# Kernel optimization log

Hardware: AMD Instinct MI355X
Metric: run time of the kernel (lower is better)

Reference implementation:

```python
import jax, jax.numpy as jnp
import numpy as np

N = 20000       # nodes
E = 160000      # edges (avg degree 8)
NFEAT = 512
NHID = 512
NCLASS = 64
NLAYERS = 4


def setup_inputs() -> dict:
    key = jax.random.key(0)
    ks = jax.random.split(key, 9)
    s = 0.05
    x = jax.random.normal(ks[0], (N, NFEAT), dtype=jnp.float32)
    edge_index = jax.random.randint(ks[1], (2, E), 0, N, dtype=jnp.int64)
    W_enc = jax.random.normal(ks[2], (NFEAT, NHID), dtype=jnp.float32) * s
    b_enc = jnp.zeros((NHID,), dtype=jnp.float32)
    W_convs = jax.random.normal(ks[3], (NLAYERS, NHID, NHID), dtype=jnp.float32) * s
    b_convs = jnp.zeros((NLAYERS, NHID), dtype=jnp.float32)
    W_dec = jax.random.normal(ks[4], (NHID, NCLASS), dtype=jnp.float32) * s
    b_dec = jnp.zeros((NCLASS,), dtype=jnp.float32)
    return {"x": x, "edge_index": edge_index, "W_enc": W_enc, "b_enc": b_enc,
            "W_convs": W_convs, "b_convs": b_convs, "W_dec": W_dec, "b_dec": b_dec}


def reference(x, edge_index, W_enc, b_enc, W_convs, b_convs, W_dec, b_dec):
    n = x.shape[0]
    loops = jnp.arange(n, dtype=edge_index.dtype)
    # GCNConv adds self-loops, then sym-normalizes: D^-1/2 (A+I) D^-1/2
    src = jnp.concatenate([edge_index[0], loops])  # [E+N]
    dst = jnp.concatenate([edge_index[1], loops])  # [E+N]
    deg = jax.ops.segment_sum(jnp.ones_like(dst, dtype=x.dtype), dst, num_segments=N)
    dinv = jnp.where(deg > 0, jax.lax.rsqrt(deg), jnp.zeros_like(deg))
    norm = (dinv[src] * dinv[dst])[:, None]  # [E+N, 1]

    # encoder: relu(Linear)
    h = jax.nn.relu(x @ W_enc + b_enc)

    def gcn_step(h, wb):
        W, b = wb
        hW = h @ W                                   # [N, H]
        msg = hW[src] * norm                         # gather + scale
        agg = jax.ops.segment_sum(msg, dst, num_segments=N)  # scatter-add
        return jax.nn.relu(agg + b), None            # bias after aggregation (PyG)

    h, _ = jax.lax.scan(gcn_step, h, (W_convs, b_convs))

    # decoder (dropout p=0 in eval -> identity)
    return h @ W_dec + b_dec
```

## Files before the change

kernel.cpp:

```cpp
#include <hip/hip_runtime.h>

#define N_NODES 20000
#define E_EDGES 160000
#define NFEAT   512
#define NHID    512
#define NCLASS  64
#define NLAYERS 4

#define SCAN_CHUNK 1024
#define NBLK ((N_NODES + SCAN_CHUNK - 1) / SCAN_CHUNK)
#define CNT_BLOCKS ((E_EDGES + 255) / 256)

using bf16x8 = __attribute__((ext_vector_type(8))) short;
using f32x4  = __attribute__((ext_vector_type(4))) float;
using u16x8  = __attribute__((ext_vector_type(8))) unsigned short;

__device__ __forceinline__ unsigned short f2bf(float f) {
    union { float f; unsigned int u; } v; v.f = f;
    unsigned int u = v.u + 0x7FFFu + ((v.u >> 16) & 1u);
    return (unsigned short)(u >> 16);
}
__device__ __forceinline__ float bf2f(unsigned short h) {
    union { unsigned int u; float f; } v; v.u = ((unsigned int)h) << 16;
    return v.f;
}
__device__ __forceinline__ void gl2lds16(const void* gptr, void* lptr) {
    __builtin_amdgcn_global_load_lds(
        (const __attribute__((address_space(1))) unsigned int*)gptr,
        (__attribute__((address_space(3))) unsigned int*)lptr,
        16, 0, 0);
}

__global__ __launch_bounds__(256) void prep_all(const int* __restrict__ dst,
                                                int* __restrict__ counts,
                                                int* __restrict__ bsums,
                                                const float* __restrict__ W_enc,
                                                const float* __restrict__ W_convs,
                                                const float* __restrict__ W_dec,
                                                unsigned short* __restrict__ WencT,
                                                unsigned short* __restrict__ WcvT,
                                                unsigned short* __restrict__ WdecT) {
    __shared__ int bins[NBLK];
    __shared__ float tile[32][33];
    const int b = blockIdx.x, t = threadIdx.x;

    if (b < CNT_BLOCKS) {
        if (t < NBLK) bins[t] = 0;
        __syncthreads();
        const int e = b * 256 + t;
        if (e < E_EDGES) {
            const int d = dst[e];
            atomicAdd(&counts[d], 1);
            atomicAdd(&bins[d >> 10], 1);
        }
        __syncthreads();
        if (t < NBLK && bins[t]) atomicAdd(&bsums[t], bins[t]);
        return;
    }

    const int bid = b - CNT_BLOCKS;
    const int id  = bid >> 8;
    const int rem = bid & 255;
    const int n0  = (rem & 15) * 32;
    const int k0  = (rem >> 4) * 32;
    const float* W; unsigned short* WT; int N;
    const int K = 512;
    if (id == 0)            { W = W_enc; WT = WencT; N = NHID; }
    else if (id <= NLAYERS) { W = W_convs + (size_t)(id - 1) * NHID * NHID;
                              WT = WcvT  + (size_t)(id - 1) * NHID * NHID; N = NHID; }
    else                    { W = W_dec; WT = WdecT; N = NCLASS; }
    if (n0 >= N) return;
    const int tx = t & 31, ty = t >> 5;
#pragma unroll
    for (int i = 0; i < 32; i += 8)
        tile[ty + i][tx] = W[(size_t)(k0 + ty + i) * N + n0 + tx];
    __syncthreads();
#pragma unroll
    for (int i = 0; i < 32; i += 8)
        WT[(size_t)(n0 + ty + i) * K + k0 + tx] = f2bf(tile[tx][ty + i]);
}

__global__ __launch_bounds__(64) void scan_bsums(const int* __restrict__ bsums,
                                                 int* __restrict__ boffs) {
    const int t = threadIdx.x;
    const int orig = (t < NBLK) ? bsums[t] : 0;
    int v = orig;
    for (int off = 1; off < 64; off <<= 1) {
        int u = __shfl_up(v, off, 64);
        if (t >= off) v += u;
    }
    if (t < NBLK) boffs[t] = v - orig;
}

__global__ __launch_bounds__(256) void write_rowptr(const int* __restrict__ counts,
                                                    const int* __restrict__ boffs,
                                                    int* __restrict__ row_ptr,
                                                    int* __restrict__ cursor,
                                                    float* __restrict__ dinv) {
    __shared__ int part[256];
    const int b = blockIdx.x, t = threadIdx.x;
    const int base = b * SCAN_CHUNK + t * 4;
    int c[4], s = 0;
    for (int i = 0; i < 4; ++i) {
        int idx = base + i;
        c[i] = (idx < N_NODES) ? counts[idx] : 0;
        s += c[i];
    }
    part[t] = s;
    __syncthreads();
    for (int off = 1; off < 256; off <<= 1) {
        int v = (t >= off) ? part[t - off] : 0;
        __syncthreads();
        part[t] += v;
        __syncthreads();
    }
    int run = boffs[b] + ((t == 0) ? 0 : part[t - 1]);
    for (int i = 0; i < 4; ++i) {
        int idx = base + i;
        if (idx < N_NODES) {
            row_ptr[idx] = run;
            cursor[idx]  = run;
            dinv[idx]    = rsqrtf((float)c[i] + 1.0f);
            run += c[i];
        }
    }
    if (b == 0 && t == 0) row_ptr[N_NODES] = E_EDGES;
}

__global__ __launch_bounds__(256) void csr_fill(const int* __restrict__ src,
                                                const int* __restrict__ dst,
                                                const float* __restrict__ dinv,
                                                int* __restrict__ cursor,
                                                int2* __restrict__ ew) {
    int e = blockIdx.x * 256 + threadIdx.x;
    if (e < E_EDGES) {
        int s = src[e], d = dst[e];
        int pos = atomicAdd(&cursor[d], 1);
        ew[pos] = make_int2(s, __float_as_int(dinv[s] * dinv[d]));
    }
    if (e < 8) ew[E_EDGES + e] = make_int2(0, 0);
}

template <int BM, int BN, int WR, int WC, bool RELU, bool HASBIAS, bool OUTBF16, bool A32>
__global__ __launch_bounds__(256) void gemm_mfma(const void* __restrict__ Aptr,
                                                 const unsigned short* __restrict__ BT,
                                                 const float* __restrict__ bias,
                                                 void* __restrict__ Cout,
                                                 int M, int N, int K) {
    constexpr int BK = 32;
    constexpr int R  = BM / (16 * WR);
    constexpr int C  = BN / (16 * WC);
    constexpr int RA = (BM * BK) / (256 * 8);
    constexpr int RB = (BN * BK) / (256 * 8);
    __shared__ unsigned short lA[BM * BK];
    __shared__ unsigned short lB[BN * BK];

    const int t    = threadIdx.x;
    const int lane = t & 63;
    const int wv   = t >> 6;
    const int wr   = wv / WC;
    const int wc   = wv % WC;
    const int lm   = lane & 15;
    const int quad = lane >> 4;

    const int MBLK = (M + BM - 1) / BM;
    const int NBN  = N / BN;
    int mblk, nblk;
    {
        const int i    = blockIdx.x;
        const int full = (MBLK / 8) * 8 * NBN;
        if (i < full) {
            const int g = i / (8 * NBN);
            const int l = i % (8 * NBN);
            mblk = g * 8 + (l & 7);
            nblk = l >> 3;
        } else {
            const int t2  = i - full;
            const int rem = MBLK - (MBLK / 8) * 8;
            mblk = (MBLK / 8) * 8 + t2 % rem;
            nblk = t2 / rem;
        }
    }
    const int m0 = mblk * BM;
    const int n0 = nblk * BN;

    f32x4 acc[R][C] = {};

    for (int kt = 0; kt < K; kt += BK) {
#pragma unroll
        for (int i = 0; i < RA; ++i) {
            int idx = i * 256 + t;
            int row = idx >> 2;
            int kof = (idx & 3) << 3;
            int gr = m0 + row; if (gr >= M) gr = M - 1;
            if constexpr (!A32) {
                gl2lds16((const unsigned short*)Aptr + (size_t)gr * K + kt + kof,
                         &lA[idx * 8]);
            } else {
                const float* p = (const float*)Aptr + (size_t)gr * K + kt + kof;
                float4 f0 = *(const float4*)p;
                float4 f1 = *(const float4*)(p + 4);
                u16x8 pk;
                pk[0] = f2bf(f0.x); pk[1] = f2bf(f0.y);
                pk[2] = f2bf(f0.z); pk[3] = f2bf(f0.w);
                pk[4] = f2bf(f1.x); pk[5] = f2bf(f1.y);
                pk[6] = f2bf(f1.z); pk[7] = f2bf(f1.w);
                *(u16x8*)&lA[idx * 8] = pk;
            }
        }
#pragma unroll
        for (int i = 0; i < RB; ++i) {
            int idx = i * 256 + t;
            int row = idx >> 2;
            int kof = (idx & 3) << 3;
            gl2lds16(BT + (size_t)(n0 + row) * K + kt + kof, &lB[idx * 8]);
        }
        __syncthreads();

        bf16x8 af[R], bfr[C];
#pragma unroll
        for (int r = 0; r < R; ++r)
            af[r] = *(const bf16x8*)&lA[(wr * R * 16 + r * 16 + lm) * BK + quad * 8];
#pragma unroll
        for (int c = 0; c < C; ++c)
            bfr[c] = *(const bf16x8*)&lB[(wc * C * 16 + c * 16 + lm) * BK + quad * 8];
#pragma unroll
        for (int r = 0; r < R; ++r)
#pragma unroll
            for (int c = 0; c < C; ++c)
                acc[r][c] = __builtin_amdgcn_mfma_f32_16x16x32_bf16(af[r], bfr[c],
                                                                    acc[r][c], 0, 0, 0);
        __syncthreads();
    }

#pragma unroll
    for (int r = 0; r < R; ++r) {
#pragma unroll
        for (int c = 0; c < C; ++c) {
            const int colg = n0 + wc * C * 16 + c * 16 + lm;
            const float bb = HASBIAS ? bias[colg] : 0.0f;
            const int rowb = m0 + wr * R * 16 + r * 16 + quad * 4;
#pragma unroll
            for (int i = 0; i < 4; ++i) {
                const int rr = rowb + i;
                if (rr < M) {
                    float v = acc[r][c][i] + bb;
                    if (RELU) v = fmaxf(v, 0.0f);
                    if (OUTBF16)
                        ((unsigned short*)Cout)[(size_t)rr * N + colg] = f2bf(v);
                    else
                        ((float*)Cout)[(size_t)rr * N + colg] = v;
                }
            }
        }
    }
}

__global__ __launch_bounds__(256) void gcn_aggregate(const unsigned short* __restrict__ hW,
                                                     const int* __restrict__ row_ptr,
                                                     const int2* __restrict__ ew,
                                                     const float* __restrict__ dinv,
                                                     const float* __restrict__ bias,
                                                     unsigned short* __restrict__ out) {
    const int wv   = threadIdx.x >> 6;
    const int lane = threadIdx.x & 63;
    int d = blockIdx.x * 4 + wv;
    d = __builtin_amdgcn_readfirstlane(d);
    if (d >= N_NODES) return;
    const int beg = __builtin_amdgcn_readfirstlane(row_ptr[d]);
    const int end = __builtin_amdgcn_readfirstlane(row_ptr[d + 1]);
    const size_t foff = (size_t)lane * 8;

    const float di = dinv[d];
    const float sl = di * di;
    u16x8 sv = *(const u16x8*)(hW + (size_t)d * NHID + foff);
    float acc[8];
#pragma unroll
    for (int i = 0; i < 8; ++i) acc[i] = bf2f(sv[i]) * sl;

    for (int j = beg; j < end; j += 8) {
        int   sK[8];
        float wK[8];
        u16x8 v[8];
#pragma unroll
        for (int k = 0; k < 8; ++k) {
            const int jj = j + k;
            const int2 e = ew[jj];
            const bool valid = jj < end;
            sK[k] = valid ? e.x : 0;
            wK[k] = valid ? __int_as_float(e.y) : 0.0f;
        }
#pragma unroll
        for (int k = 0; k < 8; ++k)
            v[k] = *(const u16x8*)(hW + (size_t)sK[k] * NHID + foff);
#pragma unroll
        for (int k = 0; k < 8; ++k)
#pragma unroll
            for (int i = 0; i < 8; ++i)
                acc[i] += bf2f(v[k][i]) * wK[k];
    }

    const float4 b0v = *(const float4*)(bias + foff);
    const float4 b1v = *(const float4*)(bias + foff + 4);
    u16x8 r;
    r[0] = f2bf(fmaxf(acc[0] + b0v.x, 0.0f));
    r[1] = f2bf(fmaxf(acc[1] + b0v.y, 0.0f));
    r[2] = f2bf(fmaxf(acc[2] + b0v.z, 0.0f));
    r[3] = f2bf(fmaxf(acc[3] + b0v.w, 0.0f));
    r[4] = f2bf(fmaxf(acc[4] + b1v.x, 0.0f));
    r[5] = f2bf(fmaxf(acc[5] + b1v.y, 0.0f));
    r[6] = f2bf(fmaxf(acc[6] + b1v.z, 0.0f));
    r[7] = f2bf(fmaxf(acc[7] + b1v.w, 0.0f));
    *(u16x8*)(out + (size_t)d * NHID + foff) = r;
}

extern "C" void kernel_launch(void* const* d_in, const int* in_sizes, int n_in,
                              void* d_out, int out_size, void* d_ws, size_t ws_size,
                              hipStream_t stream) {
    const float* x       = (const float*)d_in[0];
    const int*   ei      = (const int*)d_in[1];
    const float* W_enc   = (const float*)d_in[2];
    const float* b_enc   = (const float*)d_in[3];
    const float* W_convs = (const float*)d_in[4];
    const float* b_convs = (const float*)d_in[5];
    const float* W_dec   = (const float*)d_in[6];
    const float* b_dec   = (const float*)d_in[7];
    float* out = (float*)d_out;

    const int* src = ei;
    const int* dst = ei + E_EDGES;

    char* ws = (char*)d_ws;
    auto alloc = [&](size_t bytes) {
        char* p = ws;
        ws += (bytes + 255) / 256 * 256;
        return p;
    };
    float* dinv     = (float*)alloc(N_NODES * 4);
    int*   counts   = (int*)  alloc((N_NODES + NBLK) * 4);
    int*   bsums    = counts + N_NODES;
    int*   row_ptr  = (int*)  alloc((N_NODES + 1) * 4);
    int*   cursor   = (int*)  alloc(N_NODES * 4);
    int*   boffs    = (int*)  alloc(NBLK * 4);
    int2*  ew       = (int2*) alloc((E_EDGES + 8) * 8);
    unsigned short* WencT = (unsigned short*)alloc((size_t)NFEAT * NHID * 2);
    unsigned short* WcvT  = (unsigned short*)alloc((size_t)NLAYERS * NHID * NHID * 2);
    unsigned short* WdecT = (unsigned short*)alloc((size_t)NHID * NCLASS * 2);
    unsigned short* B1    = (unsigned short*)alloc((size_t)N_NODES * NHID * 2);
    unsigned short* B2    = (unsigned short*)alloc((size_t)N_NODES * NHID * 2);

    hipMemsetAsync(counts, 0, (N_NODES + NBLK) * sizeof(int), stream);
    prep_all<<<CNT_BLOCKS + 6 * 256, 256, 0, stream>>>(
        dst, counts, bsums, W_enc, W_convs, W_dec, WencT, WcvT, WdecT);
    scan_bsums<<<1, 64, 0, stream>>>(bsums, boffs);
    write_rowptr<<<NBLK, 256, 0, stream>>>(counts, boffs, row_ptr, cursor, dinv);
    csr_fill<<<(E_EDGES + 255) / 256, 256, 0, stream>>>(src, dst, dinv, cursor, ew);

    const int MBLK64 = (N_NODES + 63) / 64;

    gemm_mfma<64, 128, 2, 2, true, true, true, true>
        <<<MBLK64 * (NHID / 128), 256, 0, stream>>>(
        x, WencT, b_enc, B1, N_NODES, NHID, NFEAT);

    for (int L = 0; L < NLAYERS; ++L) {
        gemm_mfma<64, 128, 2, 2, false, false, true, false>
            <<<MBLK64 * (NHID / 128), 256, 0, stream>>>(
            B1, WcvT + (size_t)L * NHID * NHID, nullptr, B2, N_NODES, NHID, NHID);
        gcn_aggregate<<<(N_NODES + 3) / 4, 256, 0, stream>>>(
            B2, row_ptr, ew, dinv, b_convs + (size_t)L * NHID, B1);
    }

    gemm_mfma<64, 64, 2, 2, false, true, false, false>
        <<<MBLK64 * (NCLASS / 64), 256, 0, stream>>>(
        B1, WdecT, b_dec, out, N_NODES, NCLASS, NHID);
}
```

Baseline: 340.7 us.

## Double-buffer GEMM LDS tiles and pre-convert x to bf16 in prep kernel

The MFMA GEMM now uses two LDS buffers and issues the global-to-LDS loads for the next K tile before computing the current one. It uses explicit vmcnt waits and raw s_barrier in place of __syncthreads, so memory latency can overlap with MFMA work. The encoder's fp32 A input is now converted to bf16 once, in extra blocks of the prep kernel, into the B2 scratch buffer. This lets every GEMM take the async-load path without converting in the inner loop. The cost is twice the LDS per block, which may lower occupancy, plus an extra pass over x and fragile hand-written wait counts.

```diff
diff --git a/kernel.cpp b/kernel.cpp
--- a/kernel.cpp
+++ b/kernel.cpp
@@ -10,6 +10,7 @@
 #define SCAN_CHUNK 1024
 #define NBLK ((N_NODES + SCAN_CHUNK - 1) / SCAN_CHUNK)
 #define CNT_BLOCKS ((E_EDGES + 255) / 256)
+#define CVT_BLOCKS ((N_NODES * NFEAT) / 2048)
 
 using bf16x8 = __attribute__((ext_vector_type(8))) short;
 using f32x4  = __attribute__((ext_vector_type(4))) float;
@@ -39,7 +40,9 @@
                                                 const float* __restrict__ W_dec,
                                                 unsigned short* __restrict__ WencT,
                                                 unsigned short* __restrict__ WcvT,
-                                                unsigned short* __restrict__ WdecT) {
+                                                unsigned short* __restrict__ WdecT,
+                                                const float* __restrict__ x,
+                                                unsigned short* __restrict__ Xbf) {
     __shared__ int bins[NBLK];
     __shared__ float tile[32][33];
     const int b = blockIdx.x, t = threadIdx.x;
@@ -55,6 +58,20 @@
         }
         __syncthreads();
         if (t < NBLK && bins[t]) atomicAdd(&bsums[t], bins[t]);
+        return;
+    }
+
+    if (b >= CNT_BLOCKS + 6 * 256) {
+        const int cid = b - CNT_BLOCKS - 6 * 256;
+        const size_t base = (size_t)cid * 2048 + (size_t)t * 8;
+        const float4 f0 = *(const float4*)(x + base);
+        const float4 f1 = *(const float4*)(x + base + 4);
+        u16x8 pk;
+        pk[0] = f2bf(f0.x); pk[1] = f2bf(f0.y);
+        pk[2] = f2bf(f0.z); pk[3] = f2bf(f0.w);
+        pk[4] = f2bf(f1.x); pk[5] = f2bf(f1.y);
+        pk[6] = f2bf(f1.z); pk[7] = f2bf(f1.w);
+        *(u16x8*)(Xbf + base) = pk;
         return;
     }
 
@@ -141,19 +158,20 @@
     if (e < 8) ew[E_EDGES + e] = make_int2(0, 0);
 }
 
-template <int BM, int BN, int WR, int WC, bool RELU, bool HASBIAS, bool OUTBF16, bool A32>
-__global__ __launch_bounds__(256) void gemm_mfma(const void* __restrict__ Aptr,
+template <int BM, int BN, int WR, int WC, bool RELU, bool HASBIAS, bool OUTBF16>
+__global__ __launch_bounds__(256) void gemm_mfma(const unsigned short* __restrict__ A,
                                                  const unsigned short* __restrict__ BT,
                                                  const float* __restrict__ bias,
                                                  void* __restrict__ Cout,
                                                  int M, int N, int K) {
-    constexpr int BK = 32;
-    constexpr int R  = BM / (16 * WR);
-    constexpr int C  = BN / (16 * WC);
-    constexpr int RA = (BM * BK) / (256 * 8);
-    constexpr int RB = (BN * BK) / (256 * 8);
-    __shared__ unsigned short lA[BM * BK];
-    __shared__ unsigned short lB[BN * BK];
+    constexpr int BK  = 32;
+    constexpr int R   = BM / (16 * WR);
+    constexpr int C   = BN / (16 * WC);
+    constexpr int RA  = (BM * BK) / (256 * 8);
+    constexpr int RB  = (BN * BK) / (256 * 8);
+    constexpr int LPT = RA + RB;
+    __shared__ unsigned short lA[2][BM * BK];
+    __shared__ unsigned short lB[2][BN * BK];
 
     const int t    = threadIdx.x;
     const int lane = t & 63;
@@ -186,51 +204,54 @@
 
     f32x4 acc[R][C] = {};
 
-    for (int kt = 0; kt < K; kt += BK) {
+    auto stage = [&](int s, int kt) {
 #pragma unroll
         for (int i = 0; i < RA; ++i) {
             int idx = i * 256 + t;
             int row = idx >> 2;
             int kof = (idx & 3) << 3;
             int gr = m0 + row; if (gr >= M) gr = M - 1;
-            if constexpr (!A32) {
-                gl2lds16((const unsigned short*)Aptr + (size_t)gr * K + kt + kof,
-                         &lA[idx * 8]);
-            } else {
-                const float* p = (const float*)Aptr + (size_t)gr * K + kt + kof;
-                float4 f0 = *(const float4*)p;
-                float4 f1 = *(const float4*)(p + 4);
-                u16x8 pk;
-                pk[0] = f2bf(f0.x); pk[1] = f2bf(f0.y);
-                pk[2] = f2bf(f0.z); pk[3] = f2bf(f0.w);
-                pk[4] = f2bf(f1.x); pk[5] = f2bf(f1.y);
-                pk[6] = f2bf(f1.z); pk[7] = f2bf(f1.w);
-                *(u16x8*)&lA[idx * 8] = pk;
-            }
+            gl2lds16(A + (size_t)gr * K + kt + kof, &lA[s][idx * 8]);
         }
 #pragma unroll
         for (int i = 0; i < RB; ++i) {
             int idx = i * 256 + t;
             int row = idx >> 2;
             int kof = (idx & 3) << 3;
-            gl2lds16(BT + (size_t)(n0 + row) * K + kt + kof, &lB[idx * 8]);
-        }
-        __syncthreads();
+            gl2lds16(BT + (size_t)(n0 + row) * K + kt + kof, &lB[s][idx * 8]);
+        }
+    };
+
+    stage(0, 0);
+    int cur = 0;
+    for (int kt = 0; kt < K; kt += BK) {
+        if (kt + BK < K) {
+            stage(cur ^ 1, kt + BK);
+            asm volatile("s_waitcnt vmcnt(%0)" :: "i"(LPT) : "memory");
+        } else {
+            asm volatile("s_waitcnt vmcnt(0)" ::: "memory");
+        }
+        __builtin_amdgcn_sched_barrier(0);
+        __builtin_amdgcn_s_barrier();
 
         bf16x8 af[R], bfr[C];
 #pragma unroll
         for (int r = 0; r < R; ++r)
-            af[r] = *(const bf16x8*)&lA[(wr * R * 16 + r * 16 + lm) * BK + quad * 8];
+            af[r] = *(const bf16x8*)&lA[cur][(wr * R * 16 + r * 16 + lm) * BK + quad * 8];
 #pragma unroll
         for (int c = 0; c < C; ++c)
-            bfr[c] = *(const bf16x8*)&lB[(wc * C * 16 + c * 16 + lm) * BK + quad * 8];
+            bfr[c] = *(const bf16x8*)&lB[cur][(wc * C * 16 + c * 16 + lm) * BK + quad * 8];
+        asm volatile("s_waitcnt lgkmcnt(0)" ::: "memory");
+        __builtin_amdgcn_sched_barrier(0);
 #pragma unroll
         for (int r = 0; r < R; ++r)
 #pragma unroll
             for (int c = 0; c < C; ++c)
                 acc[r][c] = __builtin_amdgcn_mfma_f32_16x16x32_bf16(af[r], bfr[c],
                                                                     acc[r][c], 0, 0, 0);
-        __syncthreads();
+        __builtin_amdgcn_sched_barrier(0);
+        __builtin_amdgcn_s_barrier();
+        cur ^= 1;
     }
 
 #pragma unroll
@@ -348,29 +369,30 @@
     unsigned short* WdecT = (unsigned short*)alloc((size_t)NHID * NCLASS * 2);
     unsigned short* B1    = (unsigned short*)alloc((size_t)N_NODES * NHID * 2);
     unsigned short* B2    = (unsigned short*)alloc((size_t)N_NODES * NHID * 2);
+    unsigned short* Xbf   = B2;
 
     hipMemsetAsync(counts, 0, (N_NODES + NBLK) * sizeof(int), stream);
-    prep_all<<<CNT_BLOCKS + 6 * 256, 256, 0, stream>>>(
-        dst, counts, bsums, W_enc, W_convs, W_dec, WencT, WcvT, WdecT);
+    prep_all<<<CNT_BLOCKS + 6 * 256 + CVT_BLOCKS, 256, 0, stream>>>(
+        dst, counts, bsums, W_enc, W_convs, W_dec, WencT, WcvT, WdecT, x, Xbf);
     scan_bsums<<<1, 64, 0, stream>>>(bsums, boffs);
     write_rowptr<<<NBLK, 256, 0, stream>>>(counts, boffs, row_ptr, cursor, dinv);
     csr_fill<<<(E_EDGES + 255) / 256, 256, 0, stream>>>(src, dst, dinv, cursor, ew);
 
     const int MBLK64 = (N_NODES + 63) / 64;
 
-    gemm_mfma<64, 128, 2, 2, true, true, true, true>
+    gemm_mfma<64, 128, 2, 2, true, true, true>
         <<<MBLK64 * (NHID / 128), 256, 0, stream>>>(
-        x, WencT, b_enc, B1, N_NODES, NHID, NFEAT);
+        Xbf, WencT, b_enc, B1, N_NODES, NHID, NFEAT);
 
     for (int L = 0; L < NLAYERS; ++L) {
-        gemm_mfma<64, 128, 2, 2, false, false, true, false>
+        gemm_mfma<64, 128, 2, 2, false, false, true>
             <<<MBLK64 * (NHID / 128), 256, 0, stream>>>(
             B1, WcvT + (size_t)L * NHID * NHID, nullptr, B2, N_NODES, NHID, NHID);
         gcn_aggregate<<<(N_NODES + 3) / 4, 256, 0, stream>>>(
             B2, row_ptr, ew, dinv, b_convs + (size_t)L * NHID, B1);
     }
 
-    gemm_mfma<64, 64, 2, 2, false, true, false, false>
+    gemm_mfma<64, 64, 2, 2, false, true, false>
         <<<MBLK64 * (NCLASS / 64), 256, 0, stream>>>(
         B1, WdecT, b_dec, out, N_NODES, NCLASS, NHID);
 }
```

Result: no change. 336.0 us (-1.4%).
